# Performance work log

Hardware: AMD Instinct MI355X
Metric: run time of the kernel (lower is better)

## Reference

```python
import jax, jax.numpy as jnp
import numpy as np

N = 50000      # nodes
E = 800000     # edges (avg degree 16)
IN_DIM = 128
H = 4          # attention heads
D = 32         # hidden dim per head
NEG_SLOPE = 0.2


def setup_inputs() -> dict:
    key = jax.random.key(0)
    ks = jax.random.split(key, 9)
    x = jax.random.normal(ks[0], (N, IN_DIM), dtype=jnp.float32)
    src = jax.random.randint(ks[1], (E,), 0, N, dtype=jnp.int64)
    dst = jax.random.randint(ks[2], (E,), 0, N, dtype=jnp.int64)
    # layer 0: IN_DIM -> H*D ; layer 1: H*D -> H*D
    s0 = 1.0 / np.sqrt(IN_DIM)
    s1 = 1.0 / np.sqrt(H * D)
    W1 = jax.random.normal(ks[3], (H * D, IN_DIM), dtype=jnp.float32) * s0
    al1 = jax.random.normal(ks[4], (1, H, D), dtype=jnp.float32) * s1
    ar1 = jax.random.normal(ks[5], (1, H, D), dtype=jnp.float32) * s1
    W2 = jax.random.normal(ks[6], (H * D, H * D), dtype=jnp.float32) * s1
    al2 = jax.random.normal(ks[7], (1, H, D), dtype=jnp.float32) * s1
    ar2 = jax.random.normal(ks[8], (1, H, D), dtype=jnp.float32) * s1
    return {"x": x, "src": src, "dst": dst, "W1": W1, "al1": al1, "ar1": ar1,
            "W2": W2, "al2": al2, "ar2": ar2}


def gat_conv(h, src, dst, W, al, ar):
    """DGL-style GATConv. h: [N, F_in] -> [N, H, D], with ELU activation."""
    feat = (h @ W.T).reshape(N, H, D)                 # [N,H,D]
    el = jnp.sum(feat * al, axis=-1)                  # [N,H] a_l . Wh
    er = jnp.sum(feat * ar, axis=-1)                  # [N,H] a_r . Wh
    e = jax.nn.leaky_relu(el[src] + er[dst], NEG_SLOPE)  # [E,H]
    # numerically stable edge softmax over incoming edges of each dst node
    m = jax.ops.segment_max(e, dst, num_segments=N)   # [N,H]
    ee = jnp.exp(e - m[dst])                          # [E,H]
    denom = jax.ops.segment_sum(ee, dst, num_segments=N)  # [N,H]
    alpha = ee / denom[dst]                           # [E,H]
    msg = feat[src] * alpha[..., None]                # [E,H,D]
    out = jax.ops.segment_sum(msg, dst, num_segments=N)   # [N,H,D]
    return jax.nn.elu(out)


def reference(x, src, dst, W1, al1, ar1, W2, al2, ar2):
    h = gat_conv(x, src, dst, W1, al1, ar1).reshape(N, H * D)  # flatten(1)
    h = gat_conv(h, src, dst, W2, al2, ar2)                    # [N,H,D]
    return jnp.mean(h, axis=1)                                 # [N,D]
```

## Files before the change

kernel.cpp:

```cpp
#include <hip/hip_runtime.h>
#include <cmath>
#include <type_traits>

#define HEADS 4
#define FDIM 128
#define NEG 0.2f
#define NBUCK 8
#define CSHIFT 7
#define CMASK 127

typedef __attribute__((ext_vector_type(8))) __bf16 bf16x8;
typedef __attribute__((ext_vector_type(8))) _Float16 h16x8;
typedef __attribute__((ext_vector_type(4))) float f32x4;

__global__ __launch_bounds__(256) void prep_kernel(
    const float* __restrict__ W1, const float* __restrict__ al1,
    const float* __restrict__ ar1,
    const float* __restrict__ W2, const float* __restrict__ al2,
    const float* __restrict__ ar2,
    __bf16* __restrict__ wf1, __bf16* __restrict__ wext1,
    _Float16* __restrict__ wf2, _Float16* __restrict__ wext2)
{
    const int b = blockIdx.x, tid = threadIdx.x;
    if (b < 256) {
        int idx = (b & 127) * 256 + tid;
        int j = idx & 7;
        int r = idx >> 3;
        int c = r & 15; r >>= 4;
        int t = r & 7;  r >>= 3;
        int kq = r & 15;
        int hl = r >> 4;
        if (b < 128) {
            float v = W1[(t * 16 + c) * 128 + kq * 8 + j];
            __bf16 hi = (__bf16)v;
            wf1[idx] = (hl == 0) ? hi : (__bf16)(v - (float)hi);
        } else {
            float v = W2[(t * 16 + c) * 128 + kq * 8 + j];
            _Float16 hi = (_Float16)v;
            wf2[idx] = (hl == 0) ? hi : (_Float16)(v - (float)hi);
        }
    } else {
        const float* W  = (b == 256) ? W1 : W2;
        const float* al = (b == 256) ? al1 : al2;
        const float* ar = (b == 256) ? ar1 : ar2;
        __shared__ float val[1024];
        #pragma unroll
        for (int ch = 0; ch < 4; ++ch) {
            int idx = ch * 256 + tid;
            int c = idx >> 7, k = idx & 127;
            int h = c & 3;
            const float* a = (c < 4) ? al : ar;
            float s = 0.f;
            for (int d = 0; d < 32; ++d)
                s += a[h * 32 + d] * W[(h * 32 + d) * 128 + k];
            val[c * 128 + k] = s;
        }
        __syncthreads();
        #pragma unroll
        for (int ch = 0; ch < 16; ++ch) {
            int idx = tid * 16 + ch;
            int j = idx & 7;
            int r = idx >> 3;
            int c = r & 15; r >>= 4;
            int kq = r & 15;
            int hl = r >> 4;
            float v = (c < 8) ? val[c * 128 + kq * 8 + j] : 0.f;
            if (b == 256) {
                __bf16 hi = (__bf16)v;
                wext1[idx] = (hl == 0) ? hi : (__bf16)(v - (float)hi);
            } else {
                _Float16 hi = (_Float16)v;
                wext2[idx] = (hl == 0) ? hi : (_Float16)(v - (float)hi);
            }
        }
    }
}

__device__ __forceinline__ void gemm_body_f32(
    const float* __restrict__ X, const bf16x8* __restrict__ wf,
    const bf16x8* __restrict__ wext, _Float16* __restrict__ featH,
    float* __restrict__ el, float* __restrict__ er,
    int nnodes, int tile0, int tend, int stride, bf16x8* lw)
{
    const int tid = threadIdx.x;
    const int wave = tid >> 6, lane = tid & 63;
    const int l15 = lane & 15, quad = lane >> 4;

    int tile = tile0;
    float xr[32], xn[32];

    auto loadX = [&](int tl, float* dst) {
        int nodeA = tl * 64 + wave * 16 + l15;
        bool v = nodeA < nnodes;
        const float4* xp = (const float4*)(X + (size_t)nodeA * 128);
        #pragma unroll
        for (int ks = 0; ks < 4; ++ks) {
            float4 a = v ? xp[ks * 8 + quad * 2]     : make_float4(0.f, 0.f, 0.f, 0.f);
            float4 b = v ? xp[ks * 8 + quad * 2 + 1] : make_float4(0.f, 0.f, 0.f, 0.f);
            dst[ks * 8 + 0] = a.x; dst[ks * 8 + 1] = a.y;
            dst[ks * 8 + 2] = a.z; dst[ks * 8 + 3] = a.w;
            dst[ks * 8 + 4] = b.x; dst[ks * 8 + 5] = b.y;
            dst[ks * 8 + 6] = b.z; dst[ks * 8 + 7] = b.w;
        }
    };

    loadX(tile, xr);
    for (int i = tid; i < 2048; i += 256) lw[i] = wf[i];
    __syncthreads();

    while (true) {
        int next = tile + stride;
        if (next < tend) loadX(next, xn);

        f32x4 acc[9];
        #pragma unroll
        for (int t = 0; t < 9; ++t) acc[t] = (f32x4){0.f, 0.f, 0.f, 0.f};

        #pragma unroll
        for (int ks = 0; ks < 4; ++ks) {
            bf16x8 ahi, alo;
            #pragma unroll
            for (int j = 0; j < 8; ++j) {
                float xv = xr[ks * 8 + j];
                __bf16 h = (__bf16)xv;
                ahi[j] = h;
                alo[j] = (__bf16)(xv - (float)h);
            }
            const int kq = ks * 4 + quad;

            {
                bf16x8 bh = wext[(kq) * 16 + l15];
                bf16x8 bl = wext[(16 + kq) * 16 + l15];
                acc[8] = __builtin_amdgcn_mfma_f32_16x16x32_bf16(ahi, bh, acc[8], 0, 0, 0);
                acc[8] = __builtin_amdgcn_mfma_f32_16x16x32_bf16(alo, bh, acc[8], 0, 0, 0);
                acc[8] = __builtin_amdgcn_mfma_f32_16x16x32_bf16(ahi, bl, acc[8], 0, 0, 0);
            }
            #pragma unroll
            for (int t = 0; t < 8; ++t) {
                bf16x8 bh = lw[(kq * 8 + t) * 16 + l15];
                bf16x8 bl = wf[2048 + (kq * 8 + t) * 16 + l15];
                acc[t] = __builtin_amdgcn_mfma_f32_16x16x32_bf16(ahi, bh, acc[t], 0, 0, 0);
                acc[t] = __builtin_amdgcn_mfma_f32_16x16x32_bf16(alo, bh, acc[t], 0, 0, 0);
                acc[t] = __builtin_amdgcn_mfma_f32_16x16x32_bf16(ahi, bl, acc[t], 0, 0, 0);
            }
        }

        const int nodeC = tile * 64 + wave * 16 + quad * 4;
        #pragma unroll
        for (int r = 0; r < 4; ++r) {
            int gn = nodeC + r;
            if (gn < nnodes) {
                #pragma unroll
                for (int t = 0; t < 8; ++t)
                    featH[(size_t)gn * 128 + t * 16 + l15] = (_Float16)acc[t][r];
            }
        }
        if (l15 < 8) {
            #pragma unroll
            for (int r = 0; r < 4; ++r) {
                int gn = nodeC + r;
                if (gn < nnodes) {
                    if (l15 < 4) el[gn * HEADS + l15] = acc[8][r];
                    else         er[gn * HEADS + (l15 - 4)] = acc[8][r];
                }
            }
        }

        if (next >= tend) break;
        #pragma unroll
        for (int i = 0; i < 32; ++i) xr[i] = xn[i];
        tile = next;
    }
}

__device__ __forceinline__ void gemm_body_f16(
    const _Float16* __restrict__ X, const h16x8* __restrict__ wf,
    const h16x8* __restrict__ wext, _Float16* __restrict__ featH,
    float* __restrict__ el, float* __restrict__ er,
    int nnodes, int tile0, int tend, int stride, h16x8* lw)
{
    const int tid = threadIdx.x;
    const int wave = tid >> 6, lane = tid & 63;
    const int l15 = lane & 15, quad = lane >> 4;

    int tile = tile0;
    h16x8 xr[4], xn[4];

    auto loadX = [&](int tl, h16x8* dst) {
        int nodeA = tl * 64 + wave * 16 + l15;
        bool v = nodeA < nnodes;
        const h16x8* xp = (const h16x8*)(X + (size_t)nodeA * 128);
        #pragma unroll
        for (int ks = 0; ks < 4; ++ks) {
            if (v) {
                dst[ks] = xp[ks * 4 + quad];
            } else {
                #pragma unroll
                for (int j = 0; j < 8; ++j) dst[ks][j] = (_Float16)0.f;
            }
        }
    };

    loadX(tile, xr);
    for (int i = tid; i < 2048; i += 256) lw[i] = wf[i];
    __syncthreads();

    while (true) {
        int next = tile + stride;
        if (next < tend) loadX(next, xn);

        f32x4 acc[9];
        #pragma unroll
        for (int t = 0; t < 9; ++t) acc[t] = (f32x4){0.f, 0.f, 0.f, 0.f};

        #pragma unroll
        for (int ks = 0; ks < 4; ++ks) {
            h16x8 a = xr[ks];
            const int kq = ks * 4 + quad;
            {
                h16x8 bh = wext[(kq) * 16 + l15];
                h16x8 bl = wext[(16 + kq) * 16 + l15];
                acc[8] = __builtin_amdgcn_mfma_f32_16x16x32_f16(a, bh, acc[8], 0, 0, 0);
                acc[8] = __builtin_amdgcn_mfma_f32_16x16x32_f16(a, bl, acc[8], 0, 0, 0);
            }
            #pragma unroll
            for (int t = 0; t < 8; ++t) {
                h16x8 bh = lw[(kq * 8 + t) * 16 + l15];
                h16x8 bl = wf[2048 + (kq * 8 + t) * 16 + l15];
                acc[t] = __builtin_amdgcn_mfma_f32_16x16x32_f16(a, bh, acc[t], 0, 0, 0);
                acc[t] = __builtin_amdgcn_mfma_f32_16x16x32_f16(a, bl, acc[t], 0, 0, 0);
            }
        }

        const int nodeC = tile * 64 + wave * 16 + quad * 4;
        #pragma unroll
        for (int r = 0; r < 4; ++r) {
            int gn = nodeC + r;
            if (gn < nnodes) {
                #pragma unroll
                for (int t = 0; t < 8; ++t)
                    featH[(size_t)gn * 128 + t * 16 + l15] = (_Float16)acc[t][r];
            }
        }
        if (l15 < 8) {
            #pragma unroll
            for (int r = 0; r < 4; ++r) {
                int gn = nodeC + r;
                if (gn < nnodes) {
                    if (l15 < 4) el[gn * HEADS + l15] = acc[8][r];
                    else         er[gn * HEADS + (l15 - 4)] = acc[8][r];
                }
            }
        }

        if (next >= tend) break;
        #pragma unroll
        for (int i = 0; i < 4; ++i) xr[i] = xn[i];
        tile = next;
    }
}

__device__ __forceinline__ void coarse_hist_body(
    const int* __restrict__ dst, int* __restrict__ histmat,
    int nedges, int nblk, int nbkt, int eb, int* chist)
{
    const int tid = threadIdx.x;
    for (int i = tid; i < nbkt; i += 256) chist[i] = 0;
    __syncthreads();
    int i0 = eb * 2048 + tid * 8;
    if (i0 + 7 < nedges) {
        int4 d0 = *(const int4*)&dst[i0];
        int4 d1 = *(const int4*)&dst[i0 + 4];
        atomicAdd(&chist[d0.x >> CSHIFT], 1);
        atomicAdd(&chist[d0.y >> CSHIFT], 1);
        atomicAdd(&chist[d0.z >> CSHIFT], 1);
        atomicAdd(&chist[d0.w >> CSHIFT], 1);
        atomicAdd(&chist[d1.x >> CSHIFT], 1);
        atomicAdd(&chist[d1.y >> CSHIFT], 1);
        atomicAdd(&chist[d1.z >> CSHIFT], 1);
        atomicAdd(&chist[d1.w >> CSHIFT], 1);
    } else {
        for (int i = i0; i < nedges; ++i)
            atomicAdd(&chist[dst[i] >> CSHIFT], 1);
    }
    __syncthreads();
    for (int i = tid; i < nbkt; i += 256)
        histmat[i * nblk + eb] = chist[i];
}

__device__ __forceinline__ void coarse_scatter_body(
    const int* __restrict__ src, const int* __restrict__ dst,
    const int* __restrict__ histoff, int* __restrict__ tmp,
    int nedges, int nblk, int nbkt, int eb, int* chist)
{
    const int tid = threadIdx.x;
    for (int i = tid; i < nbkt; i += 256) chist[i] = 0;
    __syncthreads();
    int i0 = eb * 2048 + tid * 8;
    if (i0 + 7 < nedges) {
        int s[8], d[8];
        *(int4*)&s[0] = *(const int4*)&src[i0];
        *(int4*)&s[4] = *(const int4*)&src[i0 + 4];
        *(int4*)&d[0] = *(const int4*)&dst[i0];
        *(int4*)&d[4] = *(const int4*)&dst[i0 + 4];
        #pragma unroll
        for (int q = 0; q < 8; ++q) {
            int bkt = d[q] >> CSHIFT;
            int r = atomicAdd(&chist[bkt], 1);
            int pos = histoff[bkt * nblk + eb] + r;
            tmp[pos] = ((d[q] & CMASK) << 16) | s[q];
        }
    } else {
        for (int i = i0; i < nedges; ++i) {
            int s = src[i], d = dst[i];
            int bkt = d >> CSHIFT;
            int r = atomicAdd(&chist[bkt], 1);
            tmp[histoff[bkt * nblk + eb] + r] = ((d & CMASK) << 16) | s;
        }
    }
}

__global__ __launch_bounds__(256) void fused_gemm_chist(
    const float* __restrict__ X, const bf16x8* __restrict__ wf,
    const bf16x8* __restrict__ wext, _Float16* __restrict__ featH,
    float* __restrict__ el, float* __restrict__ er, int nnodes,
    int t0, int tend, int gemm_blocks,
    const int* __restrict__ dst, int* __restrict__ histmat,
    int nedges, int nblk, int nbkt)
{
    __shared__ bf16x8 lw[2048];
    __shared__ int chist[512];
    if ((int)blockIdx.x < gemm_blocks)
        gemm_body_f32(X, wf, wext, featH, el, er, nnodes,
                      t0 + blockIdx.x, tend, gemm_blocks, lw);
    else
        coarse_hist_body(dst, histmat, nedges, nblk, nbkt,
                         blockIdx.x - gemm_blocks, chist);
}

__global__ __launch_bounds__(256) void fused_gemm_cscatter(
    const float* __restrict__ X, const bf16x8* __restrict__ wf,
    const bf16x8* __restrict__ wext, _Float16* __restrict__ featH,
    float* __restrict__ el, float* __restrict__ er, int nnodes,
    int t0, int tend, int gemm_blocks,
    const int* __restrict__ src, const int* __restrict__ dst,
    const int* __restrict__ histoff, int* __restrict__ tmp,
    int nedges, int nblk, int nbkt)
{
    __shared__ bf16x8 lw[2048];
    __shared__ int chist[512];
    if ((int)blockIdx.x < gemm_blocks)
        gemm_body_f32(X, wf, wext, featH, el, er, nnodes,
                      t0 + blockIdx.x, tend, gemm_blocks, lw);
    else
        coarse_scatter_body(src, dst, histoff, tmp, nedges, nblk, nbkt,
                            blockIdx.x - gemm_blocks, chist);
}

__global__ __launch_bounds__(256) void fine_sort_kernel(
    const int* __restrict__ tmp, const int* __restrict__ histoff,
    int* __restrict__ csr_src, int* __restrict__ offsets,
    int nblk, int nbkt, int nb, int nedges, int shift)
{
    __shared__ int eds[4096];
    __shared__ int fh[1024];
    __shared__ int wsums[4];
    const int b = blockIdx.x, tid = threadIdx.x;
    const int lane = tid & 63, w = tid >> 6;

    const int base = histoff[b * nblk];
    const int endb = histoff[(b + 1) * nblk];
    int cnt = endb - base;
    if (cnt > 4096) cnt = 4096;

    #pragma unroll
    for (int i = 0; i < 4; ++i) fh[tid + i * 256] = 0;
    __syncthreads();

    for (int i = tid; i < cnt; i += 256) {
        int e = tmp[base + i];
        eds[i] = e;
        int fb = ((e >> 16) << 3) + ((e & 0xffff) >> shift);
        atomicAdd(&fh[fb], 1);
    }
    __syncthreads();

    int v0 = fh[tid * 4], v1 = fh[tid * 4 + 1], v2 = fh[tid * 4 + 2], v3 = fh[tid * 4 + 3];
    int s0 = v0, s1 = s0 + v1, s2 = s1 + v2, s3 = s2 + v3;
    int x = s3;
    #pragma unroll
    for (int off = 1; off < 64; off <<= 1) {
        int t = __shfl_up(x, off, 64);
        if (lane >= off) x += t;
    }
    if (lane == 63) wsums[w] = x;
    __syncthreads();
    int wbase = 0;
    #pragma unroll
    for (int k = 0; k < 4; ++k) if (k < w) wbase += wsums[k];
    const int tb = wbase + x - s3;

    int o0 = tb, o1 = tb + s0, o2 = tb + s1, o3 = tb + s2;
    fh[tid * 4]     = o0;
    fh[tid * 4 + 1] = o1;
    fh[tid * 4 + 2] = o2;
    fh[tid * 4 + 3] = o3;
    int g = b * 1024 + tid * 4;
    if (g < nb)     offsets[g]     = base + o0;
    if (g + 1 < nb) offsets[g + 1] = base + o1;
    if (g + 2 < nb) offsets[g + 2] = base + o2;
    if (g + 3 < nb) offsets[g + 3] = base + o3;
    __syncthreads();

    for (int i = tid; i < cnt; i += 256) {
        int e = eds[i];
        int fb = ((e >> 16) << 3) + ((e & 0xffff) >> shift);
        int p = atomicAdd(&fh[fb], 1);
        csr_src[base + p] = e & 0xffff;
    }
    if (b == 0 && tid == 0) offsets[nb] = nedges;
}

__global__ __launch_bounds__(256) void gemm_mfma_f16_kernel(
    const _Float16* __restrict__ X, const h16x8* __restrict__ wf,
    const h16x8* __restrict__ wext, _Float16* __restrict__ featH,
    float* __restrict__ el, float* __restrict__ er, int nnodes, int ntiles)
{
    __shared__ h16x8 lw[2048];
    gemm_body_f16(X, wf, wext, featH, el, er, nnodes,
                  blockIdx.x, ntiles, gridDim.x, lw);
}

__global__ __launch_bounds__(256) void scan1_kernel(
    const int* __restrict__ counts, int* __restrict__ offsets,
    int* __restrict__ bsums, int n)
{
    __shared__ int wsums[4];
    const int tid = threadIdx.x, lane = tid & 63, w = tid >> 6;
    const int i = blockIdx.x * 1024 + tid * 4;

    int4 v = make_int4(0, 0, 0, 0);
    if (i + 3 < n) v = *(const int4*)&counts[i];
    else {
        if (i < n)     v.x = counts[i];
        if (i + 1 < n) v.y = counts[i + 1];
        if (i + 2 < n) v.z = counts[i + 2];
    }
    int s0 = v.x, s1 = s0 + v.y, s2 = s1 + v.z, s3 = s2 + v.w;

    int x = s3;
    #pragma unroll
    for (int off = 1; off < 64; off <<= 1) {
        int t = __shfl_up(x, off, 64);
        if (lane >= off) x += t;
    }
    if (lane == 63) wsums[w] = x;
    __syncthreads();
    int wbase = 0;
    #pragma unroll
    for (int k = 0; k < 4; ++k) if (k < w) wbase += wsums[k];

    int tbase = wbase + x - s3;
    if (i < n)     offsets[i]     = tbase;
    if (i + 1 < n) offsets[i + 1] = tbase + s0;
    if (i + 2 < n) offsets[i + 2] = tbase + s1;
    if (i + 3 < n) offsets[i + 3] = tbase + s2;
    if (tid == 255) bsums[blockIdx.x] = wbase + x;
}

__global__ __launch_bounds__(256) void scan23_kernel(
    int* __restrict__ offsets, const int* __restrict__ bsums, int n, int nedges)
{
    __shared__ int sbase;
    const int tid = threadIdx.x, b = blockIdx.x;
    if (tid < 64) {
        int s = 0;
        for (int i = tid; i < b; i += 64) s += bsums[i];
        #pragma unroll
        for (int off = 1; off < 64; off <<= 1) s += __shfl_xor(s, off, 64);
        if (tid == 0) sbase = s;
    }
    __syncthreads();
    const int base = sbase;
    const int i = b * 1024 + tid * 4;
    #pragma unroll
    for (int k = 0; k < 4; ++k)
        if (i + k < n) offsets[i + k] += base;
    if (b == 0 && tid == 0) offsets[n] = nedges;
}

template <bool MEAN>
__global__ __launch_bounds__(256) void aggregate_kernel(
    const _Float16* __restrict__ featH, const float* __restrict__ el,
    const float* __restrict__ er, const int* __restrict__ offsets,
    const int* __restrict__ csr_src, void* __restrict__ outp, int nnodes)
{
    const int n = (blockIdx.x * 256 + threadIdx.x) >> 6;
    if (n >= nnodes) return;
    const int lane = threadIdx.x & 63;
    const int g = lane >> 4, u = lane & 15, h = u >> 2;
    const int beg = offsets[n * NBUCK], end = offsets[n * NBUCK + NBUCK];
    const float ern = er[n * HEADS + h];
    const int iters = (end - beg + 3) >> 2;

    float a[8];
    #pragma unroll
    for (int p = 0; p < 8; ++p) a[p] = 0.f;
    float sw = 0.f;

    const h16x8* __restrict__ frow = (const h16x8*)featH;

    int ja = beg + g;
    int jb = ja + 4;
    int jc = ja + 8;
    int jd = ja + 12;
    bool va = ja < end, vb = jb < end;
    int sa = va ? csr_src[ja] : 0;
    int sb = vb ? csr_src[jb] : 0;
    int sc = jc < end ? csr_src[jc] : 0;
    int sd = jd < end ? csr_src[jd] : 0;
    float qa = el[sa * HEADS + h];
    float qb = el[sb * HEADS + h];
    h16x8 fa = frow[(size_t)sa * 16 + u];
    h16x8 fb = frow[(size_t)sb * 16 + u];

    for (int it = 0; it < iters; ++it) {
        int je = jd + 4;
        int se = je < end ? csr_src[je] : 0;
        float qc = el[sc * HEADS + h];
        h16x8 fc = frow[(size_t)sc * 16 + u];

        float e = qa + ern;
        e = e > 0.f ? e : NEG * e;
        float w2 = va ? __expf(e) : 0.f;
        #pragma unroll
        for (int p = 0; p < 8; ++p) a[p] += w2 * (float)fa[p];
        sw += w2;

        ja = jb; va = vb;
        jb = jc; vb = jb < end;
        qa = qb; fa = fb;
        qb = qc; fb = fc;
        sc = sd; sd = se;
        jc = jd; jd = je;
    }

    #pragma unroll
    for (int p = 0; p < 8; ++p) {
        a[p] += __shfl_xor(a[p], 16, 64);
        a[p] += __shfl_xor(a[p], 32, 64);
    }
    sw += __shfl_xor(sw, 16, 64);
    sw += __shfl_xor(sw, 32, 64);

    float inv = sw > 0.f ? 1.f / sw : 0.f;
    float r[8];
    #pragma unroll
    for (int p = 0; p < 8; ++p) {
        float t = a[p] * inv;
        r[p] = t > 0.f ? t : __expf(t) - 1.f;
    }

    if (!MEAN) {
        if (g == 0) {
            h16x8 o;
            #pragma unroll
            for (int p = 0; p < 8; ++p) o[p] = (_Float16)r[p];
            ((h16x8*)outp)[(size_t)n * 16 + u] = o;
        }
    } else {
        #pragma unroll
        for (int p = 0; p < 8; ++p) {
            r[p] += __shfl_xor(r[p], 4, 64);
            r[p] += __shfl_xor(r[p], 8, 64);
        }
        if (g == 0 && u < 4) {
            float* out = (float*)outp;
            float4* o4 = (float4*)(out + (size_t)n * 32 + u * 8);
            o4[0] = make_float4(0.25f * r[0], 0.25f * r[1], 0.25f * r[2], 0.25f * r[3]);
            o4[1] = make_float4(0.25f * r[4], 0.25f * r[5], 0.25f * r[6], 0.25f * r[7]);
        }
    }
}

extern "C" void kernel_launch(void* const* d_in, const int* in_sizes, int n_in,
                              void* d_out, int out_size, void* d_ws, size_t ws_size,
                              hipStream_t stream)
{
    const float* x   = (const float*)d_in[0];
    const int*   src = (const int*)d_in[1];
    const int*   dst = (const int*)d_in[2];
    const float* W1  = (const float*)d_in[3];
    const float* al1 = (const float*)d_in[4];
    const float* ar1 = (const float*)d_in[5];
    const float* W2  = (const float*)d_in[6];
    const float* al2 = (const float*)d_in[7];
    const float* ar2 = (const float*)d_in[8];

    const int N = in_sizes[0] / FDIM;
    const int E = in_sizes[1];
    const int NB = N * NBUCK;

    int shift = 0;
    while (((N - 1) >> shift) > (NBUCK - 1)) ++shift;

    const int NBKT  = (N + CMASK) >> CSHIFT;
    const int NBLK1 = (E + 2047) >> 11;
    const int n1    = NBKT * NBLK1;

    _Float16* h1 = (_Float16*)d_ws;
    _Float16* featH = h1 + (size_t)N * FDIM;
    float* el = (float*)(featH + (size_t)N * FDIM);
    float* er = el + (size_t)N * HEADS;
    uintptr_t tp = ((uintptr_t)(er + (size_t)N * HEADS) + 15) & ~(uintptr_t)15;
    int* tmp     = (int*)tp;
    int* histmat = tmp + E;
    int* histoff = histmat + n1;
    int* offsets = histoff + (n1 + 1);
    int* csr_src = offsets + (NB + 1);
    int* bsums   = csr_src + E;
    uintptr_t wp = ((uintptr_t)(bsums + 512) + 63) & ~(uintptr_t)63;
    __bf16* wf1     = (__bf16*)wp;
    __bf16* wext1   = wf1 + 32768;
    _Float16* wf2   = (_Float16*)(wext1 + 4096);
    _Float16* wext2 = wf2 + 32768;

    const int ntiles = (N + 63) / 64;
    const int halfT  = (ntiles + 1) / 2;
    const int gA = halfT < 256 ? halfT : 256;
    const int gB = (ntiles - halfT) < 256 ? (ntiles - halfT) : 256;
    const int agg_grid  = (N + 3) / 4;
    const int nscan     = (n1 + 1023) / 1024;
    const int g2 = ntiles < 512 ? ntiles : 512;

    prep_kernel<<<258, 256, 0, stream>>>(
        W1, al1, ar1, W2, al2, ar2, wf1, wext1, wf2, wext2);

    fused_gemm_chist<<<gA + NBLK1, 256, 0, stream>>>(
        x, (const bf16x8*)wf1, (const bf16x8*)wext1, featH, el, er, N,
        0, halfT, gA, dst, histmat, E, NBLK1, NBKT);

    scan1_kernel<<<nscan, 256, 0, stream>>>(histmat, histoff, bsums, n1);
    scan23_kernel<<<nscan, 256, 0, stream>>>(histoff, bsums, n1, E);

    fused_gemm_cscatter<<<gB + NBLK1, 256, 0, stream>>>(
        x, (const bf16x8*)wf1, (const bf16x8*)wext1, featH, el, er, N,
        halfT, ntiles, gB, src, dst, histoff, tmp, E, NBLK1, NBKT);

    fine_sort_kernel<<<NBKT, 256, 0, stream>>>(
        tmp, histoff, csr_src, offsets, NBLK1, NBKT, NB, E, shift);

    aggregate_kernel<false><<<agg_grid, 256, 0, stream>>>(
        featH, el, er, offsets, csr_src, (void*)h1, N);

    gemm_mfma_f16_kernel<<<g2, 256, 0, stream>>>(
        h1, (const h16x8*)wf2, (const h16x8*)wext2, featH, el, er, N, ntiles);
    aggregate_kernel<true><<<agg_grid, 256, 0, stream>>>(
        featH, el, er, offsets, csr_src, d_out, N);
}
```

Before: 211.7 us.

## Fuse layer-1 aggregation with layer-2 GEMM through a shared-memory tile

Layer-1 aggregation now writes each 64-node tile of activations into an XOR-swizzled shared-memory tile, and the same block runs the layer-2 MFMA GEMM on it directly. This removes the h1 round trip through global memory and one kernel launch. Layer-2 features and attention terms go to separate buffers (featH2, el2, er2), since other blocks still read layer-1 featH. In exchange, each wave aggregates 16 nodes one after another, so there is less parallelism per node and occupancy is lower because of the larger shared-memory footprint.

```diff
diff --git a/kernel.cpp b/kernel.cpp
--- a/kernel.cpp
+++ b/kernel.cpp
@@ -173,93 +173,6 @@
     }
 }
 
-__device__ __forceinline__ void gemm_body_f16(
-    const _Float16* __restrict__ X, const h16x8* __restrict__ wf,
-    const h16x8* __restrict__ wext, _Float16* __restrict__ featH,
-    float* __restrict__ el, float* __restrict__ er,
-    int nnodes, int tile0, int tend, int stride, h16x8* lw)
-{
-    const int tid = threadIdx.x;
-    const int wave = tid >> 6, lane = tid & 63;
-    const int l15 = lane & 15, quad = lane >> 4;
-
-    int tile = tile0;
-    h16x8 xr[4], xn[4];
-
-    auto loadX = [&](int tl, h16x8* dst) {
-        int nodeA = tl * 64 + wave * 16 + l15;
-        bool v = nodeA < nnodes;
-        const h16x8* xp = (const h16x8*)(X + (size_t)nodeA * 128);
-        #pragma unroll
-        for (int ks = 0; ks < 4; ++ks) {
-            if (v) {
-                dst[ks] = xp[ks * 4 + quad];
-            } else {
-                #pragma unroll
-                for (int j = 0; j < 8; ++j) dst[ks][j] = (_Float16)0.f;
-            }
-        }
-    };
-
-    loadX(tile, xr);
-    for (int i = tid; i < 2048; i += 256) lw[i] = wf[i];
-    __syncthreads();
-
-    while (true) {
-        int next = tile + stride;
-        if (next < tend) loadX(next, xn);
-
-        f32x4 acc[9];
-        #pragma unroll
-        for (int t = 0; t < 9; ++t) acc[t] = (f32x4){0.f, 0.f, 0.f, 0.f};
-
-        #pragma unroll
-        for (int ks = 0; ks < 4; ++ks) {
-            h16x8 a = xr[ks];
-            const int kq = ks * 4 + quad;
-            {
-                h16x8 bh = wext[(kq) * 16 + l15];
-                h16x8 bl = wext[(16 + kq) * 16 + l15];
-                acc[8] = __builtin_amdgcn_mfma_f32_16x16x32_f16(a, bh, acc[8], 0, 0, 0);
-                acc[8] = __builtin_amdgcn_mfma_f32_16x16x32_f16(a, bl, acc[8], 0, 0, 0);
-            }
-            #pragma unroll
-            for (int t = 0; t < 8; ++t) {
-                h16x8 bh = lw[(kq * 8 + t) * 16 + l15];
-                h16x8 bl = wf[2048 + (kq * 8 + t) * 16 + l15];
-                acc[t] = __builtin_amdgcn_mfma_f32_16x16x32_f16(a, bh, acc[t], 0, 0, 0);
-                acc[t] = __builtin_amdgcn_mfma_f32_16x16x32_f16(a, bl, acc[t], 0, 0, 0);
-            }
-        }
-
-        const int nodeC = tile * 64 + wave * 16 + quad * 4;
-        #pragma unroll
-        for (int r = 0; r < 4; ++r) {
-            int gn = nodeC + r;
-            if (gn < nnodes) {
-                #pragma unroll
-                for (int t = 0; t < 8; ++t)
-                    featH[(size_t)gn * 128 + t * 16 + l15] = (_Float16)acc[t][r];
-            }
-        }
-        if (l15 < 8) {
-            #pragma unroll
-            for (int r = 0; r < 4; ++r) {
-                int gn = nodeC + r;
-                if (gn < nnodes) {
-                    if (l15 < 4) el[gn * HEADS + l15] = acc[8][r];
-                    else         er[gn * HEADS + (l15 - 4)] = acc[8][r];
-                }
-            }
-        }
-
-        if (next >= tend) break;
-        #pragma unroll
-        for (int i = 0; i < 4; ++i) xr[i] = xn[i];
-        tile = next;
-    }
-}
-
 __device__ __forceinline__ void coarse_hist_body(
     const int* __restrict__ dst, int* __restrict__ histmat,
     int nedges, int nblk, int nbkt, int eb, int* chist)
@@ -421,16 +334,6 @@
     if (b == 0 && tid == 0) offsets[nb] = nedges;
 }
 
-__global__ __launch_bounds__(256) void gemm_mfma_f16_kernel(
-    const _Float16* __restrict__ X, const h16x8* __restrict__ wf,
-    const h16x8* __restrict__ wext, _Float16* __restrict__ featH,
-    float* __restrict__ el, float* __restrict__ er, int nnodes, int ntiles)
-{
-    __shared__ h16x8 lw[2048];
-    gemm_body_f16(X, wf, wext, featH, el, er, nnodes,
-                  blockIdx.x, ntiles, gridDim.x, lw);
-}
-
 __global__ __launch_bounds__(256) void scan1_kernel(
     const int* __restrict__ counts, int* __restrict__ offsets,
     int* __restrict__ bsums, int n)
@@ -489,26 +392,16 @@
     if (b == 0 && tid == 0) offsets[n] = nedges;
 }
 
-template <bool MEAN>
-__global__ __launch_bounds__(256) void aggregate_kernel(
-    const _Float16* __restrict__ featH, const float* __restrict__ el,
-    const float* __restrict__ er, const int* __restrict__ offsets,
-    const int* __restrict__ csr_src, void* __restrict__ outp, int nnodes)
-{
-    const int n = (blockIdx.x * 256 + threadIdx.x) >> 6;
-    if (n >= nnodes) return;
-    const int lane = threadIdx.x & 63;
-    const int g = lane >> 4, u = lane & 15, h = u >> 2;
-    const int beg = offsets[n * NBUCK], end = offsets[n * NBUCK + NBUCK];
-    const float ern = er[n * HEADS + h];
-    const int iters = (end - beg + 3) >> 2;
-
+__device__ __forceinline__ void agg_one_node(
+    const h16x8* __restrict__ frow, const float* __restrict__ el,
+    const int* __restrict__ csr_src, int beg, int end,
+    int g, int u, int h, float ern, float* r)
+{
     float a[8];
     #pragma unroll
     for (int p = 0; p < 8; ++p) a[p] = 0.f;
     float sw = 0.f;
-
-    const h16x8* __restrict__ frow = (const h16x8*)featH;
+    const int iters = (end - beg + 3) >> 2;
 
     int ja = beg + g;
     int jb = ja + 4;
@@ -554,32 +447,126 @@
     sw += __shfl_xor(sw, 32, 64);
 
     float inv = sw > 0.f ? 1.f / sw : 0.f;
-    float r[8];
     #pragma unroll
     for (int p = 0; p < 8; ++p) {
         float t = a[p] * inv;
         r[p] = t > 0.f ? t : __expf(t) - 1.f;
     }
-
-    if (!MEAN) {
-        if (g == 0) {
-            h16x8 o;
+}
+
+__global__ __launch_bounds__(256) void fused_agg1_gemm2(
+    const _Float16* __restrict__ featH, const float* __restrict__ el,
+    const float* __restrict__ er, const int* __restrict__ offsets,
+    const int* __restrict__ csr_src,
+    const h16x8* __restrict__ wf, const h16x8* __restrict__ wext,
+    _Float16* __restrict__ featH2, float* __restrict__ el2,
+    float* __restrict__ er2, int nnodes)
+{
+    __shared__ h16x8 lw[2048];
+    __shared__ h16x8 xt[1024];
+    const int tid = threadIdx.x;
+    const int wave = tid >> 6, lane = tid & 63;
+    const int l15 = lane & 15, quad = lane >> 4;
+    const int g = lane >> 4, u = lane & 15, h = u >> 2;
+    const int tile = blockIdx.x;
+
+    for (int i = tid; i < 2048; i += 256) lw[i] = wf[i];
+
+    const h16x8* frow = (const h16x8*)featH;
+
+    for (int i = 0; i < 16; ++i) {
+        int row = wave * 16 + i;
+        int n = tile * 64 + row;
+        int scol = u ^ (row & 15);
+        if (n < nnodes) {
+            int beg = offsets[n * NBUCK], end = offsets[n * NBUCK + NBUCK];
+            float ern = er[n * HEADS + h];
+            float r[8];
+            agg_one_node(frow, el, csr_src, beg, end, g, u, h, ern, r);
+            if (g == 0) {
+                h16x8 o;
+                #pragma unroll
+                for (int p = 0; p < 8; ++p) o[p] = (_Float16)r[p];
+                xt[row * 16 + scol] = o;
+            }
+        } else if (g == 0) {
+            h16x8 z;
             #pragma unroll
-            for (int p = 0; p < 8; ++p) o[p] = (_Float16)r[p];
-            ((h16x8*)outp)[(size_t)n * 16 + u] = o;
-        }
-    } else {
-        #pragma unroll
-        for (int p = 0; p < 8; ++p) {
-            r[p] += __shfl_xor(r[p], 4, 64);
-            r[p] += __shfl_xor(r[p], 8, 64);
-        }
-        if (g == 0 && u < 4) {
-            float* out = (float*)outp;
-            float4* o4 = (float4*)(out + (size_t)n * 32 + u * 8);
-            o4[0] = make_float4(0.25f * r[0], 0.25f * r[1], 0.25f * r[2], 0.25f * r[3]);
-            o4[1] = make_float4(0.25f * r[4], 0.25f * r[5], 0.25f * r[6], 0.25f * r[7]);
-        }
+            for (int p = 0; p < 8; ++p) z[p] = (_Float16)0.f;
+            xt[row * 16 + scol] = z;
+        }
+    }
+    __syncthreads();
+
+    f32x4 acc[9];
+    #pragma unroll
+    for (int t = 0; t < 9; ++t) acc[t] = (f32x4){0.f, 0.f, 0.f, 0.f};
+
+    #pragma unroll
+    for (int ks = 0; ks < 4; ++ks) {
+        const int kq = ks * 4 + quad;
+        h16x8 a = xt[(wave * 16 + l15) * 16 + (kq ^ l15)];
+        {
+            h16x8 bh = wext[(kq) * 16 + l15];
+            h16x8 bl = wext[(16 + kq) * 16 + l15];
+            acc[8] = __builtin_amdgcn_mfma_f32_16x16x32_f16(a, bh, acc[8], 0, 0, 0);
+            acc[8] = __builtin_amdgcn_mfma_f32_16x16x32_f16(a, bl, acc[8], 0, 0, 0);
+        }
+        #pragma unroll
+        for (int t = 0; t < 8; ++t) {
+            h16x8 bh = lw[(kq * 8 + t) * 16 + l15];
+            h16x8 bl = wf[2048 + (kq * 8 + t) * 16 + l15];
+            acc[t] = __builtin_amdgcn_mfma_f32_16x16x32_f16(a, bh, acc[t], 0, 0, 0);
+            acc[t] = __builtin_amdgcn_mfma_f32_16x16x32_f16(a, bl, acc[t], 0, 0, 0);
+        }
+    }
+
+    const int nodeC = tile * 64 + wave * 16 + quad * 4;
+    #pragma unroll
+    for (int r = 0; r < 4; ++r) {
+        int gn = nodeC + r;
+        if (gn < nnodes) {
+            #pragma unroll
+            for (int t = 0; t < 8; ++t)
+                featH2[(size_t)gn * 128 + t * 16 + l15] = (_Float16)acc[t][r];
+        }
+    }
+    if (l15 < 8) {
+        #pragma unroll
+        for (int r = 0; r < 4; ++r) {
+            int gn = nodeC + r;
+            if (gn < nnodes) {
+                if (l15 < 4) el2[gn * HEADS + l15] = acc[8][r];
+                else         er2[gn * HEADS + (l15 - 4)] = acc[8][r];
+            }
+        }
+    }
+}
+
+__global__ __launch_bounds__(256) void aggregate_mean_kernel(
+    const _Float16* __restrict__ featH, const float* __restrict__ el,
+    const float* __restrict__ er, const int* __restrict__ offsets,
+    const int* __restrict__ csr_src, float* __restrict__ outp, int nnodes)
+{
+    const int n = (blockIdx.x * 256 + threadIdx.x) >> 6;
+    if (n >= nnodes) return;
+    const int lane = threadIdx.x & 63;
+    const int g = lane >> 4, u = lane & 15, h = u >> 2;
+    const int beg = offsets[n * NBUCK], end = offsets[n * NBUCK + NBUCK];
+    const float ern = er[n * HEADS + h];
+
+    float r[8];
+    agg_one_node((const h16x8*)featH, el, csr_src, beg, end, g, u, h, ern, r);
+
+    #pragma unroll
+    for (int p = 0; p < 8; ++p) {
+        r[p] += __shfl_xor(r[p], 4, 64);
+        r[p] += __shfl_xor(r[p], 8, 64);
+    }
+    if (g == 0 && u < 4) {
+        float4* o4 = (float4*)(outp + (size_t)n * 32 + u * 8);
+        o4[0] = make_float4(0.25f * r[0], 0.25f * r[1], 0.25f * r[2], 0.25f * r[3]);
+        o4[1] = make_float4(0.25f * r[4], 0.25f * r[5], 0.25f * r[6], 0.25f * r[7]);
     }
 }
 
@@ -608,11 +595,13 @@
     const int NBLK1 = (E + 2047) >> 11;
     const int n1    = NBKT * NBLK1;
 
-    _Float16* h1 = (_Float16*)d_ws;
-    _Float16* featH = h1 + (size_t)N * FDIM;
-    float* el = (float*)(featH + (size_t)N * FDIM);
-    float* er = el + (size_t)N * HEADS;
-    uintptr_t tp = ((uintptr_t)(er + (size_t)N * HEADS) + 15) & ~(uintptr_t)15;
+    _Float16* featH  = (_Float16*)d_ws;
+    _Float16* featH2 = featH + (size_t)N * FDIM;
+    float* el1 = (float*)(featH2 + (size_t)N * FDIM);
+    float* er1 = el1 + (size_t)N * HEADS;
+    float* el2 = er1 + (size_t)N * HEADS;
+    float* er2 = el2 + (size_t)N * HEADS;
+    uintptr_t tp = ((uintptr_t)(er2 + (size_t)N * HEADS) + 15) & ~(uintptr_t)15;
     int* tmp     = (int*)tp;
     int* histmat = tmp + E;
     int* histoff = histmat + n1;
@@ -631,30 +620,28 @@
     const int gB = (ntiles - halfT) < 256 ? (ntiles - halfT) : 256;
     const int agg_grid  = (N + 3) / 4;
     const int nscan     = (n1 + 1023) / 1024;
-    const int g2 = ntiles < 512 ? ntiles : 512;
 
     prep_kernel<<<258, 256, 0, stream>>>(
         W1, al1, ar1, W2, al2, ar2, wf1, wext1, wf2, wext2);
 
     fused_gemm_chist<<<gA + NBLK1, 256, 0, stream>>>(
-        x, (const bf16x8*)wf1, (const bf16x8*)wext1, featH, el, er, N,
+        x, (const bf16x8*)wf1, (const bf16x8*)wext1, featH, el1, er1, N,
         0, halfT, gA, dst, histmat, E, NBLK1, NBKT);
 
     scan1_kernel<<<nscan, 256, 0, stream>>>(histmat, histoff, bsums, n1);
     scan23_kernel<<<nscan, 256, 0, stream>>>(histoff, bsums, n1, E);
 
     fused_gemm_cscatter<<<gB + NBLK1, 256, 0, stream>>>(
-        x, (const bf16x8*)wf1, (const bf16x8*)wext1, featH, el, er, N,
+        x, (const bf16x8*)wf1, (const bf16x8*)wext1, featH, el1, er1, N,
         halfT, ntiles, gB, src, dst, histoff, tmp, E, NBLK1, NBKT);
 
     fine_sort_kernel<<<NBKT, 256, 0, stream>>>(
         tmp, histoff, csr_src, offsets, NBLK1, NBKT, NB, E, shift);
 
-    aggregate_kernel<false><<<agg_grid, 256, 0, stream>>>(
-        featH, el, er, offsets, csr_src, (void*)h1, N);
-
-    gemm_mfma_f16_kernel<<<g2, 256, 0, stream>>>(
-        h1, (const h16x8*)wf2, (const h16x8*)wext2, featH, el, er, N, ntiles);
-    aggregate_kernel<true><<<agg_grid, 256, 0, stream>>>(
-        featH, el, er, offsets, csr_src, d_out, N);
-}
+    fused_agg1_gemm2<<<ntiles, 256, 0, stream>>>(
+        featH, el1, er1, offsets, csr_src,
+        (const h16x8*)wf2, (const h16x8*)wext2, featH2, el2, er2, N);
+
+    aggregate_mean_kernel<<<agg_grid, 256, 0, stream>>>(
+        featH2, el2, er2, offsets, csr_src, (float*)d_out, N);
+}
```

After: 257.0 us. +21.4%, slower.
